# Kernel optimization log

Hardware: AMD Instinct MI355X
Metric: run time of the kernel (lower is better)

The kernel has to match this reference:

```python
import jax, jax.numpy as jnp
import numpy as np

HIDDEN = 512
ENC = 512

def setup_inputs() -> dict:
    key = jax.random.key(0)
    k1, k2, k3, k4, k5 = jax.random.split(key, 5)
    decoder_hidden = jax.random.normal(k1, (256, HIDDEN), dtype=jnp.float32)
    encoder_outputs = jax.random.normal(k2, (256, 1024, ENC), dtype=jnp.float32)
    s = 1.0 / np.sqrt(HIDDEN)
    W_h = jax.random.uniform(k3, (HIDDEN, HIDDEN), minval=-s, maxval=s, dtype=jnp.float32)
    W_s = jax.random.uniform(k4, (HIDDEN, ENC), minval=-s, maxval=s, dtype=jnp.float32)
    v = jax.random.uniform(k5, (1, HIDDEN), minval=-s, maxval=s, dtype=jnp.float32)
    return {"decoder_hidden": decoder_hidden, "encoder_outputs": encoder_outputs,
            "W_h": W_h, "W_s": W_s, "v": v}

def reference(decoder_hidden, encoder_outputs, W_h, W_s, v):
    # proj_h: (b, hidden); proj_s: (b, l, hidden)
    proj_h = decoder_hidden @ W_h.T
    proj_s = jnp.einsum('ble,he->blh', encoder_outputs, W_s)
    # additive score: v^T tanh(W_h h + W_s s_i) -> (b, l)
    scores = jnp.einsum('blh,h->bl', jnp.tanh(proj_h[:, None, :] + proj_s), v[0])
    alpha = jax.nn.softmax(scores, axis=-1)
    context = jnp.einsum('bl,ble->be', alpha, encoder_outputs)
    return (context, alpha)
```

## Files before the change

kernel.cpp:

```cpp
#include <hip/hip_runtime.h>
#include <hip/hip_bf16.h>

#define HID 512
#define ENCD 512
#define NB 256
#define SEQ 1024
#define LDSTR 520

typedef short bf16x8 __attribute__((ext_vector_type(8)));
typedef float floatx4 __attribute__((ext_vector_type(4)));
typedef unsigned short ushort8v __attribute__((ext_vector_type(8)));

__device__ __forceinline__ unsigned short f2bf(float f) {
    unsigned u = __builtin_bit_cast(unsigned, f);
    u += 0x7FFFu + ((u >> 16) & 1u);
    return (unsigned short)(u >> 16);
}
__device__ __forceinline__ ushort4 cvt4(float4 a) {
    return make_ushort4(f2bf(a.x), f2bf(a.y), f2bf(a.z), f2bf(a.w));
}
__device__ __forceinline__ ushort8v cvt8(float4 a, float4 b) {
    ushort8v r;
    r[0]=f2bf(a.x); r[1]=f2bf(a.y); r[2]=f2bf(a.z); r[3]=f2bf(a.w);
    r[4]=f2bf(b.x); r[5]=f2bf(b.y); r[6]=f2bf(b.z); r[7]=f2bf(b.w);
    return r;
}

__global__ __launch_bounds__(256) void prep_kernel(
    const float* __restrict__ dh,
    const float* __restrict__ W_h,
    const float* __restrict__ W_s,
    float* __restrict__ proj_h,
    unsigned short* __restrict__ Bshuf)
{
    __shared__ float sdh[2][HID];
    const int blk = blockIdx.x;
    const int t = threadIdx.x;
    const int b0 = blk * 2;

    ((float4*)&sdh[0][0])[t] = ((const float4*)(dh + (size_t)b0 * HID))[t];

    {
        const int id   = blk * 256 + t;
        const int lane = id & 63;
        const int nj   = (id >> 6) & 7;
        const int kt   = (id >> 9) & 15;
        const int wnG  = id >> 13;
        const int n = wnG * 128 + nj * 16 + (lane & 15);
        const int k = kt * 32 + (lane >> 4) * 8;
        const float* src = W_s + (size_t)n * HID + k;
        float4 s0 = *(const float4*)src;
        float4 s1 = *(const float4*)(src + 4);
        *(ushort4*)(Bshuf + (size_t)id * 8)     = cvt4(s0);
        *(ushort4*)(Bshuf + (size_t)id * 8 + 4) = cvt4(s1);
    }
    __syncthreads();

    #pragma unroll
    for (int i = 0; i < 2; ++i) {
        const int h = t + i * 256;
        const float4* wr = (const float4*)(W_h + (size_t)h * HID);
        float acc0 = 0.f, acc1 = 0.f;
        #pragma unroll 8
        for (int e4 = 0; e4 < HID / 4; ++e4) {
            float4 w  = wr[e4];
            float4 s0 = ((const float4*)&sdh[0][0])[e4];
            float4 s1 = ((const float4*)&sdh[1][0])[e4];
            acc0 += w.x * s0.x + w.y * s0.y + w.z * s0.z + w.w * s0.w;
            acc1 += w.x * s1.x + w.y * s1.y + w.z * s1.z + w.w * s1.w;
        }
        proj_h[(size_t)b0 * HID + h]       = acc0;
        proj_h[(size_t)(b0 + 1) * HID + h] = acc1;
    }
}

__global__ __launch_bounds__(512, 2) void fused_attn(
    const float* __restrict__ enc,
    const unsigned short* __restrict__ Bshuf,
    const float* __restrict__ proj_h,
    const float* __restrict__ v,
    float* __restrict__ ctx_out,
    float* __restrict__ alpha_out)
{
    __shared__ __align__(16) unsigned short sE[2][64 * LDSTR];
    __shared__ float sred[8][64];
    __shared__ float sscore[SEQ];
    __shared__ float se[64];
    __shared__ float sconst[4];

    const int t    = threadIdx.x;
    const int w    = t >> 6;
    const int lane = t & 63;
    const int ln15 = lane & 15;
    const int lk   = lane >> 4;
    const int b    = blockIdx.x;

    if (t == 0) { sconst[0] = -3.0e38f; sconst[1] = 0.f; }

    float phv[4], vv[4];
    #pragma unroll
    for (int nj = 0; nj < 4; ++nj) {
        const int n = w * 64 + nj * 16 + ln15;
        phv[nj] = proj_h[b * HID + n];
        vv[nj]  = v[n];
    }

    const unsigned short* bb0 = Bshuf + ((size_t)(w >> 1) * 8192 + lane) * 8;
    const int njo0 = (w & 1) * 4;

    const float* encB = enc + (size_t)b * SEQ * ENCD;

    {
        const float* g = encB + (size_t)w * ENCD + lane * 8;
        float4 f[16];
        #pragma unroll
        for (int p = 0; p < 8; ++p) {
            f[2*p]   = *(const float4*)(g + (size_t)p * 8 * ENCD);
            f[2*p+1] = *(const float4*)(g + (size_t)p * 8 * ENCD + 4);
        }
        #pragma unroll
        for (int p = 0; p < 8; ++p)
            *(ushort8v*)&sE[0][(p * 8 + w) * LDSTR + lane * 8] = cvt8(f[2*p], f[2*p+1]);
    }
    float C[8] = {0.f,0.f,0.f,0.f,0.f,0.f,0.f,0.f};
    __syncthreads();

    for (int ht = 0; ht < 16; ++ht) {
        const int cur = ht & 1;
        const unsigned short* sA = &sE[cur][0];
        floatx4 acc[4][4] = {};

        bf16x8 bfA[4], bfB[4];
        #pragma unroll
        for (int nj = 0; nj < 4; ++nj)
            bfA[nj] = *(const bf16x8*)(bb0 + (size_t)(njo0 + nj) * 512);

        float4 sf[16];

        #pragma unroll
        for (int kt2 = 0; kt2 < 8; ++kt2) {
            const int kt = kt2 * 2;
            #pragma unroll
            for (int nj = 0; nj < 4; ++nj)
                bfB[nj] = *(const bf16x8*)(bb0 + (size_t)((kt + 1) * 8 + njo0 + nj) * 512);
            if (kt == 2 && ht < 15) {
                const float* gn = encB + (size_t)((ht + 1) * 64 + w) * ENCD + lane * 8;
                #pragma unroll
                for (int p = 0; p < 8; ++p) {
                    sf[2*p]   = *(const float4*)(gn + (size_t)p * 8 * ENCD);
                    sf[2*p+1] = *(const float4*)(gn + (size_t)p * 8 * ENCD + 4);
                }
            }
            {
                bf16x8 af[4];
                #pragma unroll
                for (int mi = 0; mi < 4; ++mi)
                    af[mi] = *(const bf16x8*)(&sA[(mi * 16 + ln15) * LDSTR + kt * 32 + lk * 8]);
                #pragma unroll
                for (int nj = 0; nj < 4; ++nj)
                    #pragma unroll
                    for (int mi = 0; mi < 4; ++mi)
                        acc[mi][nj] = __builtin_amdgcn_mfma_f32_16x16x32_bf16(
                            af[mi], bfA[nj], acc[mi][nj], 0, 0, 0);
            }
            if (kt + 2 < 16) {
                #pragma unroll
                for (int nj = 0; nj < 4; ++nj)
                    bfA[nj] = *(const bf16x8*)(bb0 + (size_t)((kt + 2) * 8 + njo0 + nj) * 512);
            }
            {
                bf16x8 af[4];
                #pragma unroll
                for (int mi = 0; mi < 4; ++mi)
                    af[mi] = *(const bf16x8*)(&sA[(mi * 16 + ln15) * LDSTR + (kt + 1) * 32 + lk * 8]);
                #pragma unroll
                for (int nj = 0; nj < 4; ++nj)
                    #pragma unroll
                    for (int mi = 0; mi < 4; ++mi)
                        acc[mi][nj] = __builtin_amdgcn_mfma_f32_16x16x32_bf16(
                            af[mi], bfB[nj], acc[mi][nj], 0, 0, 0);
            }
        }

        if (ht < 15) {
            #pragma unroll
            for (int p = 0; p < 8; ++p)
                *(ushort8v*)&sE[1 - cur][(p * 8 + w) * LDSTR + lane * 8] = cvt8(sf[2*p], sf[2*p+1]);
        }

        #pragma unroll
        for (int mi = 0; mi < 4; ++mi) {
            #pragma unroll
            for (int r = 0; r < 4; ++r) {
                float s = 0.f;
                #pragma unroll
                for (int nj = 0; nj < 4; ++nj) {
                    float x = acc[mi][nj][r] + phv[nj];
                    float e = __expf(2.f * x);
                    s += vv[nj] * (1.f - 2.f / (e + 1.f));
                }
                s += __shfl_xor(s, 8, 64);
                s += __shfl_xor(s, 4, 64);
                s += __shfl_xor(s, 2, 64);
                s += __shfl_xor(s, 1, 64);
                if (ln15 == 0) sred[w][mi * 16 + lk * 4 + r] = s;
            }
        }
        __syncthreads();

        if (w == 0) {
            float sc = 0.f;
            #pragma unroll
            for (int g = 0; g < 8; ++g) sc += sred[g][lane];
            sscore[ht * 64 + lane] = sc;
            float mx = sc;
            #pragma unroll
            for (int m = 32; m >= 1; m >>= 1) mx = fmaxf(mx, __shfl_xor(mx, m, 64));
            const float m_old = sconst[0];
            const float m_new = fmaxf(m_old, mx);
            const float rr    = __expf(m_old - m_new);
            const float e     = __expf(sc - m_new);
            se[lane] = e;
            float es = e;
            #pragma unroll
            for (int m = 32; m >= 1; m >>= 1) es += __shfl_xor(es, m, 64);
            if (lane == 0) {
                sconst[0] = m_new;
                sconst[1] = sconst[1] * rr + es;
                sconst[2] = rr;
            }
        }
        __syncthreads();

        const float rr = sconst[2];
        #pragma unroll
        for (int j = 0; j < 8; ++j) C[j] *= rr;
        const float* gc = encB + (size_t)(ht * 64 + w) * ENCD + lane * 8;
        #pragma unroll
        for (int i = 0; i < 8; ++i) {
            const float ee = se[w + 8 * i];
            float4 u0 = *(const float4*)(gc + (size_t)i * 8 * ENCD);
            float4 u1 = *(const float4*)(gc + (size_t)i * 8 * ENCD + 4);
            C[0] += ee * u0.x; C[1] += ee * u0.y; C[2] += ee * u0.z; C[3] += ee * u0.w;
            C[4] += ee * u1.x; C[5] += ee * u1.y; C[6] += ee * u1.z; C[7] += ee * u1.w;
        }
    }

    {
        float* sctx = (float*)&sE[0][0];
        *(float4*)&sctx[w * 512 + lane * 8]     = make_float4(C[0], C[1], C[2], C[3]);
        *(float4*)&sctx[w * 512 + lane * 8 + 4] = make_float4(C[4], C[5], C[6], C[7]);
    }
    __syncthreads();
    {
        const float inv = 1.f / sconst[1];
        const float m_f = sconst[0];
        const float* sctx = (const float*)&sE[0][0];
        float ssum = 0.f;
        #pragma unroll
        for (int g = 0; g < 8; ++g) ssum += sctx[g * 512 + t];
        ctx_out[(size_t)b * HID + t] = ssum * inv;
        #pragma unroll
        for (int q = 0; q < 2; ++q) {
            const int l = q * 512 + t;
            alpha_out[(size_t)b * SEQ + l] = __expf(sscore[l] - m_f) * inv;
        }
    }
}

extern "C" void kernel_launch(void* const* d_in, const int* in_sizes, int n_in,
                              void* d_out, int out_size, void* d_ws, size_t ws_size,
                              hipStream_t stream) {
    const float* dh  = (const float*)d_in[0];
    const float* enc = (const float*)d_in[1];
    const float* W_h = (const float*)d_in[2];
    const float* W_s = (const float*)d_in[3];
    const float* v   = (const float*)d_in[4];

    float* ws = (float*)d_ws;
    float* proj_h = ws;
    unsigned short* Bshuf = (unsigned short*)(ws + 131072);

    float* ctx   = (float*)d_out;
    float* alpha = (float*)d_out + NB * HID;

    prep_kernel<<<128, 256, 0, stream>>>(dh, W_h, W_s, proj_h, Bshuf);
    fused_attn<<<NB, 512, 0, stream>>>(enc, Bshuf, proj_h, v, ctx, alpha);
}
```

Baseline: 1.104 ms.

## Reuse LDS bf16 tile for context and spread the next-tile prefetch across the k-loop

The context accumulation now reads the bf16 encoder tile already staged in LDS instead of re-reading fp32 encoder rows from global memory. This removes the second global pass over the large encoder tensor, at the cost of computing the context from bf16-rounded values. The next-tile prefetch is split into four small chunks interleaved with the MFMA k-loop, and the W_s fragments use a 4-deep register ring instead of double buffering, which lowers peak register use. A trailing barrier is added so the next iteration's writes cannot overwrite the tile while it is still being read.

```diff
diff --git a/kernel.cpp b/kernel.cpp
--- a/kernel.cpp
+++ b/kernel.cpp
@@ -24,6 +24,12 @@
     r[0]=f2bf(a.x); r[1]=f2bf(a.y); r[2]=f2bf(a.z); r[3]=f2bf(a.w);
     r[4]=f2bf(b.x); r[5]=f2bf(b.y); r[6]=f2bf(b.z); r[7]=f2bf(b.w);
     return r;
+}
+__device__ __forceinline__ float bflo(unsigned u) {
+    return __builtin_bit_cast(float, u << 16);
+}
+__device__ __forceinline__ float bfhi(unsigned u) {
+    return __builtin_bit_cast(float, u & 0xffff0000u);
 }
 
 __global__ __launch_bounds__(256) void prep_kernel(
@@ -110,17 +116,14 @@
 
     const float* encB = enc + (size_t)b * SEQ * ENCD;
 
-    {
-        const float* g = encB + (size_t)w * ENCD + lane * 8;
-        float4 f[16];
-        #pragma unroll
-        for (int p = 0; p < 8; ++p) {
-            f[2*p]   = *(const float4*)(g + (size_t)p * 8 * ENCD);
-            f[2*p+1] = *(const float4*)(g + (size_t)p * 8 * ENCD + 4);
-        }
-        #pragma unroll
-        for (int p = 0; p < 8; ++p)
-            *(ushort8v*)&sE[0][(p * 8 + w) * LDSTR + lane * 8] = cvt8(f[2*p], f[2*p+1]);
+    #pragma unroll
+    for (int j = 0; j < 4; ++j) {
+        const float* g0 = encB + (size_t)((2 * j) * 8 + w) * ENCD + lane * 8;
+        const float* g1 = encB + (size_t)((2 * j + 1) * 8 + w) * ENCD + lane * 8;
+        float4 a0 = ((const float4*)g0)[0], a1 = ((const float4*)g0)[1];
+        float4 b0 = ((const float4*)g1)[0], b1 = ((const float4*)g1)[1];
+        *(ushort8v*)&sE[0][((2 * j) * 8 + w) * LDSTR + lane * 8]     = cvt8(a0, a1);
+        *(ushort8v*)&sE[0][((2 * j + 1) * 8 + w) * LDSTR + lane * 8] = cvt8(b0, b1);
     }
     float C[8] = {0.f,0.f,0.f,0.f,0.f,0.f,0.f,0.f};
     __syncthreads();
@@ -128,64 +131,58 @@
     for (int ht = 0; ht < 16; ++ht) {
         const int cur = ht & 1;
         const unsigned short* sA = &sE[cur][0];
+        unsigned short* sW = &sE[1 - cur][0];
         floatx4 acc[4][4] = {};
 
-        bf16x8 bfA[4], bfB[4];
-        #pragma unroll
-        for (int nj = 0; nj < 4; ++nj)
-            bfA[nj] = *(const bf16x8*)(bb0 + (size_t)(njo0 + nj) * 512);
-
-        float4 sf[16];
-
-        #pragma unroll
-        for (int kt2 = 0; kt2 < 8; ++kt2) {
-            const int kt = kt2 * 2;
+        bf16x8 bq[4][4];
+        #pragma unroll
+        for (int s = 0; s < 4; ++s)
             #pragma unroll
             for (int nj = 0; nj < 4; ++nj)
-                bfB[nj] = *(const bf16x8*)(bb0 + (size_t)((kt + 1) * 8 + njo0 + nj) * 512);
-            if (kt == 2 && ht < 15) {
-                const float* gn = encB + (size_t)((ht + 1) * 64 + w) * ENCD + lane * 8;
-                #pragma unroll
-                for (int p = 0; p < 8; ++p) {
-                    sf[2*p]   = *(const float4*)(gn + (size_t)p * 8 * ENCD);
-                    sf[2*p+1] = *(const float4*)(gn + (size_t)p * 8 * ENCD + 4);
+                bq[s][nj] = *(const bf16x8*)(bb0 + (size_t)(s * 8 + njo0 + nj) * 512);
+
+        const bool pf = (ht < 15);
+        const float* gn = encB + (size_t)((ht + 1) * 64 + w) * ENCD + lane * 8;
+        float4 s0a, s0b, s1a, s1b;
+        if (pf) {
+            s0a = ((const float4*)gn)[0];
+            s0b = ((const float4*)gn)[1];
+            s1a = ((const float4*)(gn + (size_t)8 * ENCD))[0];
+            s1b = ((const float4*)(gn + (size_t)8 * ENCD))[1];
+        }
+
+        #pragma unroll
+        for (int kt = 0; kt < 16; ++kt) {
+            if (pf && (kt & 3) == 3) {
+                const int j = kt >> 2;
+                *(ushort8v*)&sW[((2 * j) * 8 + w) * LDSTR + lane * 8]     = cvt8(s0a, s0b);
+                *(ushort8v*)&sW[((2 * j + 1) * 8 + w) * LDSTR + lane * 8] = cvt8(s1a, s1b);
+                if (j < 3) {
+                    const float* gj = gn + (size_t)(2 * (j + 1)) * 8 * ENCD;
+                    s0a = ((const float4*)gj)[0];
+                    s0b = ((const float4*)gj)[1];
+                    s1a = ((const float4*)(gj + (size_t)8 * ENCD))[0];
+                    s1b = ((const float4*)(gj + (size_t)8 * ENCD))[1];
                 }
             }
-            {
-                bf16x8 af[4];
+
+            bf16x8 af[4];
+            #pragma unroll
+            for (int mi = 0; mi < 4; ++mi)
+                af[mi] = *(const bf16x8*)(&sA[(mi * 16 + ln15) * LDSTR + kt * 32 + lk * 8]);
+
+            #pragma unroll
+            for (int nj = 0; nj < 4; ++nj)
                 #pragma unroll
                 for (int mi = 0; mi < 4; ++mi)
-                    af[mi] = *(const bf16x8*)(&sA[(mi * 16 + ln15) * LDSTR + kt * 32 + lk * 8]);
+                    acc[mi][nj] = __builtin_amdgcn_mfma_f32_16x16x32_bf16(
+                        af[mi], bq[kt & 3][nj], acc[mi][nj], 0, 0, 0);
+
+            if (kt + 4 < 16) {
                 #pragma unroll
                 for (int nj = 0; nj < 4; ++nj)
-                    #pragma unroll
-                    for (int mi = 0; mi < 4; ++mi)
-                        acc[mi][nj] = __builtin_amdgcn_mfma_f32_16x16x32_bf16(
-                            af[mi], bfA[nj], acc[mi][nj], 0, 0, 0);
-            }
-            if (kt + 2 < 16) {
-                #pragma unroll
-                for (int nj = 0; nj < 4; ++nj)
-                    bfA[nj] = *(const bf16x8*)(bb0 + (size_t)((kt + 2) * 8 + njo0 + nj) * 512);
-            }
-            {
-                bf16x8 af[4];
-                #pragma unroll
-                for (int mi = 0; mi < 4; ++mi)
-                    af[mi] = *(const bf16x8*)(&sA[(mi * 16 + ln15) * LDSTR + (kt + 1) * 32 + lk * 8]);
-                #pragma unroll
-                for (int nj = 0; nj < 4; ++nj)
-                    #pragma unroll
-                    for (int mi = 0; mi < 4; ++mi)
-                        acc[mi][nj] = __builtin_amdgcn_mfma_f32_16x16x32_bf16(
-                            af[mi], bfB[nj], acc[mi][nj], 0, 0, 0);
-            }
-        }
-
-        if (ht < 15) {
-            #pragma unroll
-            for (int p = 0; p < 8; ++p)
-                *(ushort8v*)&sE[1 - cur][(p * 8 + w) * LDSTR + lane * 8] = cvt8(sf[2*p], sf[2*p+1]);
+                    bq[kt & 3][nj] = *(const bf16x8*)(bb0 + (size_t)((kt + 4) * 8 + njo0 + nj) * 512);
+            }
         }
 
         #pragma unroll
@@ -232,18 +229,22 @@
         }
         __syncthreads();
 
-        const float rr = sconst[2];
-        #pragma unroll
-        for (int j = 0; j < 8; ++j) C[j] *= rr;
-        const float* gc = encB + (size_t)(ht * 64 + w) * ENCD + lane * 8;
-        #pragma unroll
-        for (int i = 0; i < 8; ++i) {
-            const float ee = se[w + 8 * i];
-            float4 u0 = *(const float4*)(gc + (size_t)i * 8 * ENCD);
-            float4 u1 = *(const float4*)(gc + (size_t)i * 8 * ENCD + 4);
-            C[0] += ee * u0.x; C[1] += ee * u0.y; C[2] += ee * u0.z; C[3] += ee * u0.w;
-            C[4] += ee * u1.x; C[5] += ee * u1.y; C[6] += ee * u1.z; C[7] += ee * u1.w;
-        }
+        {
+            const float rr = sconst[2];
+            #pragma unroll
+            for (int j = 0; j < 8; ++j) C[j] *= rr;
+            #pragma unroll
+            for (int i = 0; i < 8; ++i) {
+                const int r = w + 8 * i;
+                const float ee = se[r];
+                uint4 u = *(const uint4*)&sA[r * LDSTR + lane * 8];
+                C[0] += ee * bflo(u.x); C[1] += ee * bfhi(u.x);
+                C[2] += ee * bflo(u.y); C[3] += ee * bfhi(u.y);
+                C[4] += ee * bflo(u.z); C[5] += ee * bfhi(u.z);
+                C[6] += ee * bflo(u.w); C[7] += ee * bfhi(u.w);
+            }
+        }
+        __syncthreads();
     }
 
     {
```

Result: faster. 1.020 ms (-7.5%).
